# Kernel tuning notes

Hardware: AMD Instinct MI355X
Metric: run time of the kernel (lower is better)

Reference implementation:

```python
import jax, jax.numpy as jnp
import numpy as np

E, H, F, LE, LD, K, CD, DIN = 256, 8, 1024, 4, 3, 8, 4, 4
B, S = 16, 512
SIG2 = 1.0 ** 2 + 1e-8   # dr_sigma**2 + 1e-8
EPS = 1e-5               # LayerNorm / BatchNorm eps


def _ln(x, w, b):
    m = x.mean(-1, keepdims=True)
    v = ((x - m) ** 2).mean(-1, keepdims=True)
    return (x - m) / jnp.sqrt(v + EPS) * w + b


def _gelu(x):
    return jax.nn.gelu(x, approximate=False)  # torch nn.GELU default = exact erf


def _mha(xq, xkv, qkv_w, qkv_b, out_w, out_b, bias=None):
    # torch nn.MultiheadAttention (batch_first), additive float attn bias broadcast over heads
    wq, wk, wv = jnp.split(qkv_w, 3, axis=0)
    bq, bk, bv = jnp.split(qkv_b, 3)
    q = xq @ wq.T + bq
    k = xkv @ wk.T + bk
    v = xkv @ wv.T + bv
    Bn, Tq, Tk = q.shape[0], q.shape[1], k.shape[1]
    hd = E // H
    qh = q.reshape(Bn, Tq, H, hd)
    kh = k.reshape(Bn, Tk, H, hd)
    vh = v.reshape(Bn, Tk, H, hd)
    s = jnp.einsum('bqhd,bkhd->bhqk', qh, kh) / jnp.sqrt(jnp.asarray(hd, q.dtype))
    if bias is not None:
        s = s + bias[:, None]  # same bias for every head
    p = jax.nn.softmax(s, axis=-1)
    o = jnp.einsum('bhqk,bkhd->bqhd', p, vh).reshape(Bn, Tq, E)
    return o @ out_w.T + out_b


def _forward(x, mask, parent_idx, in_w, in_b, bn_w, bn_b, dr_gamma,
             e_qkv_w, e_qkv_b, e_out_w, e_out_b, e_l1_w, e_l1_b, e_l2_w, e_l2_b,
             e_n1_w, e_n1_b, e_n2_w, e_n2_b,
             parent_w, parent_b, query_embed, c1_w, c1_b, c2_w, c2_b,
             d_sqkv_w, d_sqkv_b, d_sout_w, d_sout_b,
             d_cqkv_w, d_cqkv_b, d_cout_w, d_cout_b,
             d_l1_w, d_l1_b, d_l2_w, d_l2_b,
             d_n1_w, d_n1_b, d_n2_w, d_n2_b, d_n3_w, d_n3_b,
             child_w, child_b, o1_w, o1_b, o2_w, o2_b):
    x = jnp.nan_to_num(x)
    # input_dim==4 convention: (log_pt, dEta, dPhi, log_E)
    coords = jnp.stack([x[..., 1], x[..., 2]], axis=-1)          # [B,S,2]
    # input_proj: Linear -> BatchNorm1d (eval: mean 0, var 1) -> GELU (dropout=identity in eval)
    h = x @ in_w.T + in_b
    h = (h / jnp.sqrt(1.0 + EPS)) * bn_w + bn_b
    h = _gelu(h)
    # dR Gaussian attention bias: [B,S,S]; mask is all-valid so no -inf fill
    d = coords[:, :, None, :] - coords[:, None, :, :]
    dr2 = d[..., 0] ** 2 + d[..., 1] ** 2
    bias = -(dr_gamma[0] * dr2) / (2.0 * SIG2)
    # dR-biased pre-norm encoder
    for i in range(LE):
        hn = _ln(h, e_n1_w[i], e_n1_b[i])
        h = h + _mha(hn, hn, e_qkv_w[i], e_qkv_b[i], e_out_w[i], e_out_b[i], bias)
        hn = _ln(h, e_n2_w[i], e_n2_b[i])
        h = h + _gelu(hn @ e_l1_w[i].T + e_l1_b[i]) @ e_l2_w[i].T + e_l2_b[i]
    memory = jnp.nan_to_num(h)
    parent_logit = (memory @ parent_w.T + parent_b)[..., 0]       # [B,S]
    # conditional decoder queries
    p = memory[jnp.arange(memory.shape[0]), parent_idx]           # [B,E]
    m = mask.astype(memory.dtype)
    g = (memory * m[..., None]).sum(1) / jnp.maximum(m.sum(1, keepdims=True), 1.0)
    cond = _gelu(jnp.concatenate([p, g], -1) @ c1_w.T + c1_b) @ c2_w.T + c2_b
    t = query_embed[None] + cond[:, None]                         # [B,K,E]
    # pre-norm transformer decoder (self-attn, cross-attn, ff)
    for i in range(LD):
        tn = _ln(t, d_n1_w[i], d_n1_b[i])
        t = t + _mha(tn, tn, d_sqkv_w[i], d_sqkv_b[i], d_sout_w[i], d_sout_b[i])
        tn = _ln(t, d_n2_w[i], d_n2_b[i])
        t = t + _mha(tn, memory, d_cqkv_w[i], d_cqkv_b[i], d_cout_w[i], d_cout_b[i])
        tn = _ln(t, d_n3_w[i], d_n3_b[i])
        t = t + _gelu(tn @ d_l1_w[i].T + d_l1_b[i]) @ d_l2_w[i].T + d_l2_b[i]
    child_feat = t @ child_w.T + child_b                          # [B,K,CD]
    obj_logit = (_gelu(t @ o1_w.T + o1_b) @ o2_w.T + o2_b)[..., 0]  # [B,K]
    return parent_logit, child_feat, obj_logit


def setup_inputs() -> dict:
    key = jax.random.key(0)
    ks = iter(jax.random.split(key, 64))
    def w(shape, scale=0.05):
        return jax.random.normal(next(ks), shape, jnp.float32) * scale
    return {
        'x': jax.random.normal(next(ks), (B, S, DIN), jnp.float32),
        'mask': jnp.ones((B, S), dtype=bool),
        'parent_idx': jax.random.randint(next(ks), (B,), 0, S),
        'in_w': w((E, DIN)), 'in_b': jnp.zeros((E,)),
        'bn_w': jnp.ones((E,)), 'bn_b': jnp.zeros((E,)),
        'dr_gamma': jnp.ones((1,)),
        'e_qkv_w': w((LE, 3 * E, E)), 'e_qkv_b': jnp.zeros((LE, 3 * E)),
        'e_out_w': w((LE, E, E)), 'e_out_b': jnp.zeros((LE, E)),
        'e_l1_w': w((LE, F, E)), 'e_l1_b': jnp.zeros((LE, F)),
        'e_l2_w': w((LE, E, F)), 'e_l2_b': jnp.zeros((LE, E)),
        'e_n1_w': jnp.ones((LE, E)), 'e_n1_b': jnp.zeros((LE, E)),
        'e_n2_w': jnp.ones((LE, E)), 'e_n2_b': jnp.zeros((LE, E)),
        'parent_w': w((1, E)), 'parent_b': jnp.zeros((1,)),
        'query_embed': w((K, E), 0.02),
        'c1_w': w((E, 2 * E)), 'c1_b': jnp.zeros((E,)),
        'c2_w': w((E, E)), 'c2_b': jnp.zeros((E,)),
        'd_sqkv_w': w((LD, 3 * E, E)), 'd_sqkv_b': jnp.zeros((LD, 3 * E)),
        'd_sout_w': w((LD, E, E)), 'd_sout_b': jnp.zeros((LD, E)),
        'd_cqkv_w': w((LD, 3 * E, E)), 'd_cqkv_b': jnp.zeros((LD, 3 * E)),
        'd_cout_w': w((LD, E, E)), 'd_cout_b': jnp.zeros((LD, E)),
        'd_l1_w': w((LD, F, E)), 'd_l1_b': jnp.zeros((LD, F)),
        'd_l2_w': w((LD, E, F)), 'd_l2_b': jnp.zeros((LD, E)),
        'd_n1_w': jnp.ones((LD, E)), 'd_n1_b': jnp.zeros((LD, E)),
        'd_n2_w': jnp.ones((LD, E)), 'd_n2_b': jnp.zeros((LD, E)),
        'd_n3_w': jnp.ones((LD, E)), 'd_n3_b': jnp.zeros((LD, E)),
        'child_w': w((CD, E)), 'child_b': jnp.zeros((CD,)),
        'o1_w': w((E, E)), 'o1_b': jnp.zeros((E,)),
        'o2_w': w((1, E)), 'o2_b': jnp.zeros((1,)),
    }


def reference(x, mask, parent_idx, in_w, in_b, bn_w, bn_b, dr_gamma,
              e_qkv_w, e_qkv_b, e_out_w, e_out_b, e_l1_w, e_l1_b, e_l2_w, e_l2_b,
              e_n1_w, e_n1_b, e_n2_w, e_n2_b,
              parent_w, parent_b, query_embed, c1_w, c1_b, c2_w, c2_b,
              d_sqkv_w, d_sqkv_b, d_sout_w, d_sout_b,
              d_cqkv_w, d_cqkv_b, d_cout_w, d_cout_b,
              d_l1_w, d_l1_b, d_l2_w, d_l2_b,
              d_n1_w, d_n1_b, d_n2_w, d_n2_b, d_n3_w, d_n3_b,
              child_w, child_b, o1_w, o1_b, o2_w, o2_b):
    return _forward(x, mask, parent_idx, in_w, in_b, bn_w, bn_b, dr_gamma,
                    e_qkv_w, e_qkv_b, e_out_w, e_out_b, e_l1_w, e_l1_b, e_l2_w, e_l2_b,
                    e_n1_w, e_n1_b, e_n2_w, e_n2_b,
                    parent_w, parent_b, query_embed, c1_w, c1_b, c2_w, c2_b,
                    d_sqkv_w, d_sqkv_b, d_sout_w, d_sout_b,
                    d_cqkv_w, d_cqkv_b, d_cout_w, d_cout_b,
                    d_l1_w, d_l1_b, d_l2_w, d_l2_b,
                    d_n1_w, d_n1_b, d_n2_w, d_n2_b, d_n3_w, d_n3_b,
                    child_w, child_b, o1_w, o1_b, o2_w, o2_b)
```

## Files before the change

### kernel.cpp

```cpp
#include <hip/hip_runtime.h>
#include <math.h>

#define E 256
#define H 8
#define HD 32
#define FF 1024
#define LE 4
#define LDN 3
#define KQ 8
#define CDIM 4
#define DIN 4
#define BATCH 16
#define SEQ 512

typedef __attribute__((ext_vector_type(8))) short s8b;
typedef __attribute__((ext_vector_type(4))) float f32x4;

__device__ __forceinline__ float gelu_f(float x) {
  return 0.5f * x * (1.f + erff(x * 0.70710678118654752f));
}

__device__ __forceinline__ unsigned short f2b(float f) {
  union { float f; unsigned u; } a;
  a.f = f;
  unsigned r = (a.u + 0x7fffu + ((a.u >> 16) & 1u)) >> 16;
  return (unsigned short)r;
}

__device__ __forceinline__ float b2f(unsigned short u) {
  union { unsigned u; float f; } a;
  a.u = ((unsigned)u) << 16;
  return a.f;
}

__device__ __forceinline__ void gload16(const unsigned short* g, unsigned short* l) {
  __builtin_amdgcn_global_load_lds((const __attribute__((address_space(1))) void*)g,
                                   (__attribute__((address_space(3))) void*)l, 16, 0, 0);
}

template <int GELU, int RESID, int OMODE>
__global__ __launch_bounds__(256) void mfma_gemm_kernel(
    const unsigned short* __restrict__ A, const unsigned short* __restrict__ Wt,
    const float* __restrict__ bias, const float* __restrict__ resid,
    float* __restrict__ outf, unsigned short* __restrict__ outb,
    unsigned short* __restrict__ vtb,
    int M, int N, int K) {
  __shared__ __align__(16) unsigned short As[128 * 32];
  __shared__ __align__(16) unsigned short Bs[128 * 32];
  int tid = threadIdx.x;
  int lane = tid & 63, w = tid >> 6;
  int row0 = blockIdx.y * 128, col0 = blockIdx.x * 128;
  int wr = (w >> 1) * 64, wc = (w & 1) * 64;
  f32x4 acc[4][4] = {};

  int sr0 = w * 32 + (lane >> 2);
  int sr1 = sr0 + 16;
  int sc = lane & 3;
  int gc0 = (sc ^ ((sr0 >> 1) & 3)) * 8;
  int gc1 = (sc ^ ((sr1 >> 1) & 3)) * 8;
  const unsigned short* Ap0 = A + (size_t)(row0 + sr0) * K + gc0;
  const unsigned short* Ap1 = A + (size_t)(row0 + sr1) * K + gc1;
  const unsigned short* Bp0 = Wt + (size_t)(col0 + sr0) * K + gc0;
  const unsigned short* Bp1 = Wt + (size_t)(col0 + sr1) * K + gc1;
  unsigned short* lA0 = As + (w * 32) * 32;
  unsigned short* lA1 = As + (w * 32 + 16) * 32;
  unsigned short* lB0 = Bs + (w * 32) * 32;
  unsigned short* lB1 = Bs + (w * 32 + 16) * 32;

  for (int k0 = 0; k0 < K; k0 += 32) {
    __syncthreads();
    gload16(Ap0 + k0, lA0);
    gload16(Ap1 + k0, lA1);
    gload16(Bp0 + k0, lB0);
    gload16(Bp1 + k0, lB1);
    __syncthreads();
    int krow = lane & 15, kq = lane >> 4;
    s8b afr[4], bfr[4];
    #pragma unroll
    for (int mi = 0; mi < 4; ++mi) {
      int r = wr + mi * 16 + krow;
      afr[mi] = *(const s8b*)(As + r * 32 + ((kq ^ ((r >> 1) & 3)) * 8));
    }
    #pragma unroll
    for (int ni = 0; ni < 4; ++ni) {
      int r = wc + ni * 16 + krow;
      bfr[ni] = *(const s8b*)(Bs + r * 32 + ((kq ^ ((r >> 1) & 3)) * 8));
    }
    #pragma unroll
    for (int mi = 0; mi < 4; ++mi)
      #pragma unroll
      for (int ni = 0; ni < 4; ++ni)
        acc[mi][ni] = __builtin_amdgcn_mfma_f32_16x16x32_bf16(afr[mi], bfr[ni], acc[mi][ni], 0, 0, 0);
  }

  int cl = lane & 15, rb = (lane >> 4) * 4;
  #pragma unroll
  for (int ni = 0; ni < 4; ++ni) {
    int col = col0 + wc + ni * 16 + cl;
    float bv = bias[col];
    #pragma unroll
    for (int mi = 0; mi < 4; ++mi) {
      #pragma unroll
      for (int j = 0; j < 4; ++j) {
        int row = row0 + wr + mi * 16 + rb + j;
        float v = acc[mi][ni][j] + bv;
        if (RESID) v += resid[(size_t)row * N + col];
        if (GELU) v = gelu_f(v);
        if (OMODE == 0) {
          outf[(size_t)row * N + col] = v;
        } else if (OMODE == 1) {
          outb[(size_t)row * N + col] = f2b(v);
        } else {
          int b = row >> 9, s = row & 511;
          int sect = col >> 8, hh = (col >> 5) & 7, d = col & 31;
          if (sect < 2)
            outb[((((size_t)sect * BATCH + b) * H + hh) * SEQ + s) * HD + d] = f2b(v);
          else
            vtb[(((size_t)b * H + hh) * HD + d) * SEQ + s] = f2b(v);
        }
      }
    }
  }
}

__global__ __launch_bounds__(256) void mfma_attn_kernel(
    const unsigned short* __restrict__ qkb, const unsigned short* __restrict__ vt,
    const float2* __restrict__ carr, const float* __restrict__ gamma_p,
    unsigned short* __restrict__ out) {
  __shared__ __align__(16) unsigned short P[4][16 * 64];
  int tid = threadIdx.x, lane = tid & 63, w = tid >> 6;
  int qt = blockIdx.x, h = blockIdx.y, b = blockIdx.z;
  int q0 = qt * 64 + w * 16;
  const unsigned short* qh = qkb + (((size_t)b * H + h) * SEQ) * HD;
  const unsigned short* kh = qkb + ((((size_t)BATCH + b) * H + h) * SEQ) * HD;
  const unsigned short* vh = vt + (((size_t)b * H + h) * HD) * SEQ;
  int r16 = lane & 15, q4 = lane >> 4;
  s8b qa = *(const s8b*)(qh + (size_t)(q0 + r16) * HD + q4 * 8);
  float eq[4], pq[4];
  #pragma unroll
  for (int j = 0; j < 4; ++j) {
    float2 c = carr[b * SEQ + q0 + q4 * 4 + j];
    eq[j] = c.x; pq[j] = c.y;
  }
  float gam = gamma_p[0] * 0.49999999500000004f;
  const float scale = 0.17677669529663687f;
  float m[4], lsum[4];
  #pragma unroll
  for (int j = 0; j < 4; ++j) { m[j] = -1e30f; lsum[j] = 0.f; }
  f32x4 o0 = {}, o1 = {};
  const f32x4 zf = {0.f, 0.f, 0.f, 0.f};
  unsigned short* pw = &P[w][0];

  for (int t = 0; t < SEQ / 64; ++t) {
    int k0 = t * 64;
    f32x4 sf[4];
    #pragma unroll
    for (int f = 0; f < 4; ++f) {
      s8b bk = *(const s8b*)(kh + (size_t)(k0 + f * 16 + r16) * HD + q4 * 8);
      sf[f] = __builtin_amdgcn_mfma_f32_16x16x32_bf16(qa, bk, zf, 0, 0, 0);
    }
    float ek[4], pk[4];
    #pragma unroll
    for (int f = 0; f < 4; ++f) {
      float2 c = carr[b * SEQ + k0 + f * 16 + r16];
      ek[f] = c.x; pk[f] = c.y;
    }
    float sc_[4][4];
    float tmax[4] = {-1e30f, -1e30f, -1e30f, -1e30f};
    #pragma unroll
    for (int f = 0; f < 4; ++f)
      #pragma unroll
      for (int j = 0; j < 4; ++j) {
        float de = eq[j] - ek[f], dp = pq[j] - pk[f];
        float v = sf[f][j] * scale - gam * (de * de + dp * dp);
        sc_[f][j] = v;
        tmax[j] = fmaxf(tmax[j], v);
      }
    #pragma unroll
    for (int j = 0; j < 4; ++j) {
      #pragma unroll
      for (int off = 1; off < 16; off <<= 1)
        tmax[j] = fmaxf(tmax[j], __shfl_xor(tmax[j], off));
      float mn = fmaxf(m[j], tmax[j]);
      float al = __expf(m[j] - mn);
      m[j] = mn;
      lsum[j] *= al;
      o0[j] *= al;
      o1[j] *= al;
    }
    __syncthreads();
    #pragma unroll
    for (int f = 0; f < 4; ++f)
      #pragma unroll
      for (int j = 0; j < 4; ++j) {
        float p = __expf(sc_[f][j] - m[j]);
        lsum[j] += p;
        int prow = q4 * 4 + j;
        int c = f * 16 + r16;
        int chunk = (c >> 3) ^ (prow & 7);
        pw[prow * 64 + chunk * 8 + (c & 7)] = f2b(p);
      }
    __syncthreads();
    #pragma unroll
    for (int ks = 0; ks < 2; ++ks) {
      int chunk = (ks * 4 + q4) ^ (r16 & 7);
      s8b pa = *(const s8b*)(pw + r16 * 64 + chunk * 8);
      s8b v0 = *(const s8b*)(vh + (size_t)r16 * SEQ + k0 + ks * 32 + q4 * 8);
      s8b v1 = *(const s8b*)(vh + (size_t)(16 + r16) * SEQ + k0 + ks * 32 + q4 * 8);
      o0 = __builtin_amdgcn_mfma_f32_16x16x32_bf16(pa, v0, o0, 0, 0, 0);
      o1 = __builtin_amdgcn_mfma_f32_16x16x32_bf16(pa, v1, o1, 0, 0, 0);
    }
  }
  #pragma unroll
  for (int j = 0; j < 4; ++j) {
    #pragma unroll
    for (int off = 1; off < 16; off <<= 1)
      lsum[j] += __shfl_xor(lsum[j], off);
    float inv = 1.f / lsum[j];
    size_t rbase = ((size_t)(b * SEQ + q0 + q4 * 4 + j)) * E + h * HD;
    out[rbase + r16] = f2b(o0[j] * inv);
    out[rbase + 16 + r16] = f2b(o1[j] * inv);
  }
}

__global__ void coords_kernel(const float* __restrict__ x, float2* __restrict__ carr) {
  int i = blockIdx.x * 256 + threadIdx.x;
  if (i >= BATCH * SEQ) return;
  carr[i] = make_float2(x[(size_t)i * DIN + 1], x[(size_t)i * DIN + 2]);
}

__global__ void f2b_kernel(const float* __restrict__ in, unsigned short* __restrict__ out, int n4) {
  int i = blockIdx.x * 256 + threadIdx.x;
  if (i >= n4) return;
  float4 v = ((const float4*)in)[i];
  ushort4 o;
  o.x = f2b(v.x); o.y = f2b(v.y); o.z = f2b(v.z); o.w = f2b(v.w);
  ((ushort4*)out)[i] = o;
}

__global__ void kvw_remap_kernel(const float* __restrict__ w, const float* __restrict__ b,
                                 unsigned short* __restrict__ wout, float* __restrict__ bout) {
  int i = blockIdx.x * 256 + threadIdx.x;
  if (i < 1536) bout[i] = b[(i >> 9) * 768 + 256 + (i & 511)];
  if (i >= 98304) return;
  int row = i >> 6, cc = i & 63;
  int l = row >> 9, rr = row & 511;
  const float* src = w + ((size_t)l * 768 + 256 + rr) * 256 + cc * 4;
  float4 v = *(const float4*)src;
  ushort4 o;
  o.x = f2b(v.x); o.y = f2b(v.y); o.z = f2b(v.z); o.w = f2b(v.w);
  *(ushort4*)(wout + (size_t)row * 256 + cc * 4) = o;
}


template <int N, int GELU>
__global__ __launch_bounds__(256) void dec_ln_gemv_kernel(
    const float* __restrict__ t, const float* __restrict__ nw, const float* __restrict__ nb,
    const float* __restrict__ W, const float* __restrict__ bias, float* __restrict__ outg) {
  __shared__ float X[8][256];
  __shared__ float Pp[4][64][9];
  int b = blockIdx.x, by = blockIdx.y, tid = threadIdx.x;
  const float* tg = t + (size_t)b * 2048;
  int w = tid >> 6, l = tid & 63;
  #pragma unroll
  for (int rr = 0; rr < 2; ++rr) {
    int r = w * 2 + rr;
    float v0 = tg[r * 256 + l], v1 = tg[r * 256 + 64 + l];
    float v2 = tg[r * 256 + 128 + l], v3 = tg[r * 256 + 192 + l];
    float s = v0 + v1 + v2 + v3;
    for (int o = 32; o > 0; o >>= 1) s += __shfl_xor(s, o);
    float mean = s * (1.f / 256);
    float d0 = v0 - mean, d1 = v1 - mean, d2 = v2 - mean, d3 = v3 - mean;
    float var = d0 * d0 + d1 * d1 + d2 * d2 + d3 * d3;
    for (int o = 32; o > 0; o >>= 1) var += __shfl_xor(var, o);
    float inv = rsqrtf(var * (1.f / 256) + 1e-5f);
    X[r][l] = d0 * inv * nw[l] + nb[l];
    X[r][l + 64] = d1 * inv * nw[l + 64] + nb[l + 64];
    X[r][l + 128] = d2 * inv * nw[l + 128] + nb[l + 128];
    X[r][l + 192] = d3 * inv * nw[l + 192] + nb[l + 192];
  }
  __syncthreads();
  int j = tid & 63, kq = tid >> 6;
  int col = by * 64 + j;
  const float4* wp = (const float4*)(W + (size_t)col * 256 + kq * 64);
  float acc[8] = {};
  #pragma unroll
  for (int kk = 0; kk < 16; ++kk) {
    float4 wv = wp[kk];
    int base = kq * 64 + kk * 4;
    #pragma unroll
    for (int r = 0; r < 8; ++r) {
      float4 xv = *(const float4*)&X[r][base];
      acc[r] += xv.x * wv.x + xv.y * wv.y + xv.z * wv.z + xv.w * wv.w;
    }
  }
  #pragma unroll
  for (int r = 0; r < 8; ++r) Pp[kq][j][r] = acc[r];
  __syncthreads();
  for (int i = tid; i < 512; i += 256) {
    int r = i & 7, j2 = i >> 3;
    float v = Pp[0][j2][r] + Pp[1][j2][r] + Pp[2][j2][r] + Pp[3][j2][r] + bias[by * 64 + j2];
    if (GELU) v = gelu_f(v);
    outg[((size_t)b * 8 + r) * N + by * 64 + j2] = v;
  }
}

__global__ __launch_bounds__(256) void dec_gemv_resid_kernel(
    const float* __restrict__ Xg, const float* __restrict__ W, const float* __restrict__ bias,
    float* __restrict__ t) {
  __shared__ float X[8][256];
  __shared__ float Pp[4][64][9];
  int b = blockIdx.x, by = blockIdx.y, tid = threadIdx.x;
  const float* xg = Xg + (size_t)b * 2048;
  for (int i = tid; i < 2048; i += 256) ((float*)X)[i] = xg[i];
  __syncthreads();
  int j = tid & 63, kq = tid >> 6;
  int col = by * 64 + j;
  const float4* wp = (const float4*)(W + (size_t)col * 256 + kq * 64);
  float acc[8] = {};
  #pragma unroll
  for (int kk = 0; kk < 16; ++kk) {
    float4 wv = wp[kk];
    int base = kq * 64 + kk * 4;
    #pragma unroll
    for (int r = 0; r < 8; ++r) {
      float4 xv = *(const float4*)&X[r][base];
      acc[r] += xv.x * wv.x + xv.y * wv.y + xv.z * wv.z + xv.w * wv.w;
    }
  }
  #pragma unroll
  for (int r = 0; r < 8; ++r) Pp[kq][j][r] = acc[r];
  __syncthreads();
  for (int i = tid; i < 512; i += 256) {
    int r = i & 7, j2 = i >> 3;
    float v = Pp[0][j2][r] + Pp[1][j2][r] + Pp[2][j2][r] + Pp[3][j2][r] + bias[by * 64 + j2];
    t[((size_t)b * 8 + r) * 256 + by * 64 + j2] += v;
  }
}

__global__ __launch_bounds__(256) void dec_ffn2_kernel(
    const float* __restrict__ MIDg, const float* __restrict__ W, const float* __restrict__ bias,
    float* __restrict__ t) {
  __shared__ float X[8][1024];
  __shared__ float Pp[4][64][9];
  int b = blockIdx.x, by = blockIdx.y, tid = threadIdx.x;
  const float* xg = MIDg + (size_t)b * 8192;
  for (int i = tid; i < 8192; i += 256) ((float*)X)[i] = xg[i];
  __syncthreads();
  int j = tid & 63, kq = tid >> 6;
  int col = by * 64 + j;
  const float4* wp = (const float4*)(W + (size_t)col * 1024 + kq * 256);
  float acc[8] = {};
  #pragma unroll 8
  for (int kk = 0; kk < 64; ++kk) {
    float4 wv = wp[kk];
    int base = kq * 256 + kk * 4;
    #pragma unroll
    for (int r = 0; r < 8; ++r) {
      float4 xv = *(const float4*)&X[r][base];
      acc[r] += xv.x * wv.x + xv.y * wv.y + xv.z * wv.z + xv.w * wv.w;
    }
  }
  #pragma unroll
  for (int r = 0; r < 8; ++r) Pp[kq][j][r] = acc[r];
  __syncthreads();
  for (int i = tid; i < 512; i += 256) {
    int r = i & 7, j2 = i >> 3;
    float v = Pp[0][j2][r] + Pp[1][j2][r] + Pp[2][j2][r] + Pp[3][j2][r] + bias[by * 64 + j2];
    t[((size_t)b * 8 + r) * 256 + by * 64 + j2] += v;
  }
}

__global__ __launch_bounds__(256) void dec_selfattn_kernel(
    const float* __restrict__ qkvg, float* __restrict__ ao) {
  __shared__ float QK[8][768];
  __shared__ float S[512];
  int b = blockIdx.x, tid = threadIdx.x;
  const float* qg = qkvg + (size_t)b * 8 * 768;
  for (int i = tid; i < 6144; i += 256) ((float*)QK)[i] = qg[i];
  __syncthreads();
  for (int t2 = tid; t2 < 512; t2 += 256) {
    int h = t2 >> 6, q = (t2 >> 3) & 7, k = t2 & 7;
    const float* qp = &QK[q][h * 32];
    const float* kp = &QK[k][256 + h * 32];
    float d = 0.f;
    #pragma unroll
    for (int jj = 0; jj < 32; ++jj) d += qp[jj] * kp[jj];
    S[t2] = d * 0.17677669529663687f;
  }
  __syncthreads();
  if (tid < 64) {
    float* row = &S[tid * 8];
    float m = row[0];
    #pragma unroll
    for (int k = 1; k < 8; ++k) m = fmaxf(m, row[k]);
    float sum = 0.f;
    #pragma unroll
    for (int k = 0; k < 8; ++k) { float e = __expf(row[k] - m); row[k] = e; sum += e; }
    float inv = 1.f / sum;
    #pragma unroll
    for (int k = 0; k < 8; ++k) row[k] *= inv;
  }
  __syncthreads();
  for (int i = tid; i < 2048; i += 256) {
    int q = i >> 8, c = i & 255, h = c >> 5;
    const float* pr = &S[h * 64 + q * 8];
    float acc = 0.f;
    #pragma unroll
    for (int k = 0; k < 8; ++k) acc += pr[k] * QK[k][512 + c];
    ao[(size_t)b * 2048 + i] = acc;
  }
}

__global__ __launch_bounds__(256) void cross_attn_kernel(
    const float* __restrict__ Q, const unsigned short* __restrict__ KV,
    int koff, int voff, float* __restrict__ out) {
  __shared__ float sv[512];
  __shared__ float red[256];
  __shared__ float qv[32];
  __shared__ float pvred[8][32];
  int tid = threadIdx.x;
  int bid = blockIdx.x;
  int q = bid % KQ;
  int h = (bid / KQ) % H;
  int b = bid / (KQ * H);
  if (tid < 32) qv[tid] = Q[((size_t)(b * KQ + q)) * E + h * HD + tid];
  __syncthreads();
  const float scale = 0.17677669529663687f;
  for (int k = tid; k < SEQ; k += 256) {
    const unsigned short* kp = KV + ((size_t)(b * SEQ + k)) * 1536 + koff + h * HD;
    float d = 0.f;
    #pragma unroll
    for (int j4 = 0; j4 < 4; ++j4) {
      s8b kv8 = *(const s8b*)(kp + j4 * 8);
      #pragma unroll
      for (int j = 0; j < 8; ++j)
        d += qv[j4 * 8 + j] * b2f((unsigned short)kv8[j]);
    }
    sv[k] = d * scale;
  }
  __syncthreads();
  float m = -1e30f;
  for (int k = tid; k < SEQ; k += 256) m = fmaxf(m, sv[k]);
  red[tid] = m; __syncthreads();
  for (int s = 128; s > 0; s >>= 1) {
    if (tid < s) red[tid] = fmaxf(red[tid], red[tid + s]);
    __syncthreads();
  }
  m = red[0]; __syncthreads();
  float lsum = 0.f;
  for (int k = tid; k < SEQ; k += 256) { float e = __expf(sv[k] - m); sv[k] = e; lsum += e; }
  red[tid] = lsum; __syncthreads();
  for (int s = 128; s > 0; s >>= 1) {
    if (tid < s) red[tid] += red[tid + s];
    __syncthreads();
  }
  float denom = red[0];
  int d = tid & 31, g = tid >> 5;
  float acc = 0.f;
  for (int k = g; k < SEQ; k += 8)
    acc += sv[k] * b2f(KV[((size_t)(b * SEQ + k)) * 1536 + voff + h * HD + d]);
  pvred[g][d] = acc;
  __syncthreads();
  if (tid < 32) {
    float r = 0.f;
    #pragma unroll
    for (int gg = 0; gg < 8; ++gg) r += pvred[gg][tid];
    out[((size_t)(b * KQ + q)) * E + h * HD + tid] = r / denom;
  }
}

__global__ void ln_bf16_kernel(const float* __restrict__ in, const float* __restrict__ w,
                               const float* __restrict__ b, unsigned short* __restrict__ out) {
  int r = blockIdx.x;
  int l = threadIdx.x;
  const float* p = in + (size_t)r * E;
  float v0 = p[l], v1 = p[l + 64], v2 = p[l + 128], v3 = p[l + 192];
  float s = v0 + v1 + v2 + v3;
  for (int off = 32; off > 0; off >>= 1) s += __shfl_xor(s, off);
  float mean = s * (1.f / E);
  float d0 = v0 - mean, d1 = v1 - mean, d2 = v2 - mean, d3 = v3 - mean;
  float var = d0 * d0 + d1 * d1 + d2 * d2 + d3 * d3;
  for (int off = 32; off > 0; off >>= 1) var += __shfl_xor(var, off);
  float inv = rsqrtf(var * (1.f / E) + 1e-5f);
  unsigned short* o = out + (size_t)r * E;
  o[l]       = f2b(d0 * inv * w[l]       + b[l]);
  o[l + 64]  = f2b(d1 * inv * w[l + 64]  + b[l + 64]);
  o[l + 128] = f2b(d2 * inv * w[l + 128] + b[l + 128]);
  o[l + 192] = f2b(d3 * inv * w[l + 192] + b[l + 192]);
}

__global__ void input_proj_kernel(const float* __restrict__ x, const float* __restrict__ in_w,
                                  const float* __restrict__ in_b, const float* __restrict__ bn_w,
                                  const float* __restrict__ bn_b, float* __restrict__ h) {
  int idx = blockIdx.x * 256 + threadIdx.x;
  int row = idx >> 8, e = idx & 255;
  const float* xr = x + (size_t)row * DIN;
  float v = in_b[e];
  #pragma unroll
  for (int i = 0; i < DIN; ++i) v += xr[i] * in_w[e * DIN + i];
  v = v * (1.0f / sqrtf(1.0f + 1e-5f)) * bn_w[e] + bn_b[e];
  h[idx] = gelu_f(v);
}

__global__ __launch_bounds__(256) void pool_gather_kernel(
    const float* __restrict__ mem, const int* __restrict__ pidx, float* __restrict__ pg) {
  __shared__ float red[8][32];
  int b = blockIdx.x, cy = blockIdx.y, tid = threadIdx.x;
  int c = cy * 32 + (tid & 31), g = tid >> 5;
  float s = 0.f;
  for (int r = g; r < SEQ; r += 8)
    s += mem[((size_t)b * SEQ + r) * E + c];
  red[g][tid & 31] = s;
  __syncthreads();
  if (tid < 32) {
    float t = 0.f;
    #pragma unroll
    for (int g2 = 0; g2 < 8; ++g2) t += red[g2][tid];
    pg[(size_t)b * 512 + 256 + cy * 32 + tid] = t * (1.f / SEQ);
    pg[(size_t)b * 512 + cy * 32 + tid] = mem[((size_t)b * SEQ + pidx[b]) * E + cy * 32 + tid];
  }
}

__global__ void cond_kernel(const float* __restrict__ pg, const float* __restrict__ c1w,
                            const float* __restrict__ c1b, const float* __restrict__ c2w,
                            const float* __restrict__ c2b, const float* __restrict__ qe,
                            float* __restrict__ t) {
  __shared__ float PG[512];
  __shared__ float C1[256];
  int b = blockIdx.x, c = threadIdx.x;
  PG[c] = pg[(size_t)b * 512 + c];
  PG[c + 256] = pg[(size_t)b * 512 + 256 + c];
  __syncthreads();
  const float4* wp = (const float4*)(c1w + (size_t)c * 512);
  float acc = c1b[c];
  #pragma unroll 8
  for (int kk = 0; kk < 128; ++kk) {
    float4 wv = wp[kk];
    int base = kk * 4;
    acc += PG[base] * wv.x + PG[base + 1] * wv.y + PG[base + 2] * wv.z + PG[base + 3] * wv.w;
  }
  C1[c] = gelu_f(acc);
  __syncthreads();
  const float4* wp2 = (const float4*)(c2w + (size_t)c * 256);
  float acc2 = c2b[c];
  #pragma unroll 8
  for (int kk = 0; kk < 64; ++kk) {
    float4 wv = wp2[kk];
    int base = kk * 4;
    acc2 += C1[base] * wv.x + C1[base + 1] * wv.y + C1[base + 2] * wv.z + C1[base + 3] * wv.w;
  }
  #pragma unroll
  for (int k = 0; k < KQ; ++k)
    t[((size_t)b * KQ + k) * E + c] = qe[k * E + c] + acc2;
}

__global__ void head_kernel(const float* __restrict__ t,
                            const float* __restrict__ childw, const float* __restrict__ childb,
                            const float* __restrict__ o1w, const float* __restrict__ o1b,
                            const float* __restrict__ o2w, const float* __restrict__ o2b,
                            float* __restrict__ out_child, float* __restrict__ out_obj) {
  __shared__ float tr[256];
  __shared__ float red[256];
  int r = blockIdx.x, c = threadIdx.x;
  tr[c] = t[(size_t)r * E + c];
  __syncthreads();
  const float4* wp = (const float4*)(o1w + (size_t)c * 256);
  float acc = o1b[c];
  #pragma unroll 8
  for (int kk = 0; kk < 64; ++kk) {
    float4 wv = wp[kk];
    int base = kk * 4;
    acc += tr[base] * wv.x + tr[base + 1] * wv.y + tr[base + 2] * wv.z + tr[base + 3] * wv.w;
  }
  red[c] = gelu_f(acc) * o2w[c];
  __syncthreads();
  for (int s = 128; s > 0; s >>= 1) {
    if (c < s) red[c] += red[c + s];
    __syncthreads();
  }
  if (c == 0) out_obj[r] = red[0] + o2b[0];
  __syncthreads();
  #pragma unroll
  for (int j = 0; j < CDIM; ++j) {
    red[c] = tr[c] * childw[j * E + c];
    __syncthreads();
    for (int s = 128; s > 0; s >>= 1) {
      if (c < s) red[c] += red[c + s];
      __syncthreads();
    }
    if (c == 0) out_child[r * CDIM + j] = red[0] + childb[j];
    __syncthreads();
  }
}

__global__ void rowdot_kernel(const float* __restrict__ A, const float* __restrict__ w,
                              const float* __restrict__ bias, float* __restrict__ out) {
  int r = blockIdx.x, l = threadIdx.x;
  const float* p = A + (size_t)r * E;
  float s = p[l] * w[l] + p[l + 64] * w[l + 64] + p[l + 128] * w[l + 128] + p[l + 192] * w[l + 192];
  for (int off = 32; off > 0; off >>= 1) s += __shfl_xor(s, off);
  if (l == 0) out[r] = s + bias[0];
}

extern "C" void kernel_launch(void* const* d_in, const int* in_sizes, int n_in,
                              void* d_out, int out_size, void* d_ws, size_t ws_size,
                              hipStream_t stream) {
  const float* x          = (const float*)d_in[0];
  const int*   parent_idx = (const int*)d_in[2];
  const float* in_w  = (const float*)d_in[3];
  const float* in_b  = (const float*)d_in[4];
  const float* bn_w  = (const float*)d_in[5];
  const float* bn_b  = (const float*)d_in[6];
  const float* dr_gamma = (const float*)d_in[7];
  const float* e_qkv_w = (const float*)d_in[8];
  const float* e_qkv_b = (const float*)d_in[9];
  const float* e_out_w = (const float*)d_in[10];
  const float* e_out_b = (const float*)d_in[11];
  const float* e_l1_w = (const float*)d_in[12];
  const float* e_l1_b = (const float*)d_in[13];
  const float* e_l2_w = (const float*)d_in[14];
  const float* e_l2_b = (const float*)d_in[15];
  const float* e_n1_w = (const float*)d_in[16];
  const float* e_n1_b = (const float*)d_in[17];
  const float* e_n2_w = (const float*)d_in[18];
  const float* e_n2_b = (const float*)d_in[19];
  const float* parent_w = (const float*)d_in[20];
  const float* parent_b = (const float*)d_in[21];
  const float* query_embed = (const float*)d_in[22];
  const float* c1_w = (const float*)d_in[23];
  const float* c1_b = (const float*)d_in[24];
  const float* c2_w = (const float*)d_in[25];
  const float* c2_b = (const float*)d_in[26];
  const float* d_sqkv_w = (const float*)d_in[27];
  const float* d_sqkv_b = (const float*)d_in[28];
  const float* d_sout_w = (const float*)d_in[29];
  const float* d_sout_b = (const float*)d_in[30];
  const float* d_cqkv_w = (const float*)d_in[31];
  const float* d_cqkv_b = (const float*)d_in[32];
  const float* d_cout_w = (const float*)d_in[33];
  const float* d_cout_b = (const float*)d_in[34];
  const float* d_l1_w = (const float*)d_in[35];
  const float* d_l1_b = (const float*)d_in[36];
  const float* d_l2_w = (const float*)d_in[37];
  const float* d_l2_b = (const float*)d_in[38];
  const float* d_n1_w = (const float*)d_in[39];
  const float* d_n1_b = (const float*)d_in[40];
  const float* d_n2_w = (const float*)d_in[41];
  const float* d_n2_b = (const float*)d_in[42];
  const float* d_n3_w = (const float*)d_in[43];
  const float* d_n3_b = (const float*)d_in[44];
  const float* child_w = (const float*)d_in[45];
  const float* child_b = (const float*)d_in[46];
  const float* o1_w = (const float*)d_in[47];
  const float* o1_b = (const float*)d_in[48];
  const float* o2_w = (const float*)d_in[49];
  const float* o2_b = (const float*)d_in[50];

  float* out = (float*)d_out;
  const int ROWS = BATCH * SEQ;
  const int TROWS = BATCH * KQ;

  float* ws = (float*)d_ws;
  float* h         = ws;
  float* attnout_d = h + (size_t)ROWS * E;
  float* pg        = attnout_d + (size_t)TROWS * E;
  float* tbuf      = pg + BATCH * 2 * E;
  float* q_t       = tbuf + (size_t)TROWS * E;
  float* qkv_t     = q_t + (size_t)TROWS * E;
  float* dmid      = qkv_t + (size_t)TROWS * 3 * E;
  float* kvb3      = dmid + (size_t)TROWS * FF;
  unsigned short* kv_bf   = (unsigned short*)(kvb3 + 1536);
  unsigned short* hn_bf   = kv_bf + (size_t)ROWS * 1536;
  unsigned short* attn_bf = hn_bf + (size_t)ROWS * E;
  unsigned short* mid_bf  = attn_bf + (size_t)ROWS * E;
  unsigned short* eqkv_bf = mid_bf + (size_t)ROWS * FF;
  unsigned short* eout_bf = eqkv_bf + (size_t)LE * 3 * E * E;
  unsigned short* el1_bf  = eout_bf + (size_t)LE * E * E;
  unsigned short* el2_bf  = el1_bf + (size_t)LE * FF * E;
  unsigned short* kvw_bf  = el2_bf + (size_t)LE * E * FF;
  float2* carr = (float2*)(kvw_bf + (size_t)1536 * 256);
  unsigned short* qkb = mid_bf;
  unsigned short* vtb = mid_bf + (size_t)2 * ROWS * E;

  auto cvt = [&](const float* src, unsigned short* dst, size_t n) {
    int n4 = (int)(n / 4);
    f2b_kernel<<<(n4 + 255) / 256, 256, 0, stream>>>(src, dst, n4);
  };

  cvt(e_qkv_w, eqkv_bf, (size_t)LE * 3 * E * E);
  cvt(e_out_w, eout_bf, (size_t)LE * E * E);
  cvt(e_l1_w, el1_bf, (size_t)LE * FF * E);
  cvt(e_l2_w, el2_bf, (size_t)LE * E * FF);
  kvw_remap_kernel<<<384, 256, 0, stream>>>(d_cqkv_w, d_cqkv_b, kvw_bf, kvb3);
  coords_kernel<<<(BATCH * SEQ + 255) / 256, 256, 0, stream>>>(x, carr);

  input_proj_kernel<<<ROWS, 256, 0, stream>>>(x, in_w, in_b, bn_w, bn_b, h);

  for (int i = 0; i < LE; ++i) {
    const float* qb = e_qkv_b + (size_t)i * 3 * E;
    const float* ob = e_out_b + (size_t)i * E;
    const float* l1b = e_l1_b + (size_t)i * FF;
    const float* l2b = e_l2_b + (size_t)i * E;
    ln_bf16_kernel<<<ROWS, 64, 0, stream>>>(h, e_n1_w + i * E, e_n1_b + i * E, hn_bf);
    mfma_gemm_kernel<0, 0, 2><<<dim3(6, 64), 256, 0, stream>>>(
        hn_bf, eqkv_bf + (size_t)i * 3 * E * E, qb, nullptr, nullptr, qkb, vtb, ROWS, 3 * E, E);
    mfma_attn_kernel<<<dim3(SEQ / 64, H, BATCH), 256, 0, stream>>>(qkb, vtb, carr, dr_gamma, attn_bf);
    mfma_gemm_kernel<0, 1, 0><<<dim3(2, 64), 256, 0, stream>>>(
        attn_bf, eout_bf + (size_t)i * E * E, ob, h, h, nullptr, nullptr, ROWS, E, E);
    ln_bf16_kernel<<<ROWS, 64, 0, stream>>>(h, e_n2_w + i * E, e_n2_b + i * E, hn_bf);
    mfma_gemm_kernel<1, 0, 1><<<dim3(8, 64), 256, 0, stream>>>(
        hn_bf, el1_bf + (size_t)i * FF * E, l1b, nullptr, nullptr, mid_bf, nullptr, ROWS, FF, E);
    mfma_gemm_kernel<0, 1, 0><<<dim3(2, 64), 256, 0, stream>>>(
        mid_bf, el2_bf + (size_t)i * E * FF, l2b, h, h, nullptr, nullptr, ROWS, E, FF);
  }

  rowdot_kernel<<<ROWS, 64, 0, stream>>>(h, parent_w, parent_b, out);

  pool_gather_kernel<<<dim3(BATCH, 8), 256, 0, stream>>>(h, parent_idx, pg);
  cond_kernel<<<BATCH, 256, 0, stream>>>(pg, c1_w, c1_b, c2_w, c2_b, query_embed, tbuf);

  cvt(h, hn_bf, (size_t)ROWS * E);
  mfma_gemm_kernel<0, 0, 1><<<dim3(12, 64), 256, 0, stream>>>(
      hn_bf, kvw_bf, kvb3, nullptr, nullptr, kv_bf, nullptr, ROWS, 3 * E * 2, E);

  for (int i = 0; i < LDN; ++i) {
    dec_ln_gemv_kernel<768, 0><<<dim3(BATCH, 12), 256, 0, stream>>>(
        tbuf, d_n1_w + i * E, d_n1_b + i * E,
        d_sqkv_w + (size_t)i * 3 * E * E, d_sqkv_b + (size_t)i * 3 * E, qkv_t);
    dec_selfattn_kernel<<<BATCH, 256, 0, stream>>>(qkv_t, attnout_d);
    dec_gemv_resid_kernel<<<dim3(BATCH, 4), 256, 0, stream>>>(
        attnout_d, d_sout_w + (size_t)i * E * E, d_sout_b + (size_t)i * E, tbuf);
    dec_ln_gemv_kernel<256, 0><<<dim3(BATCH, 4), 256, 0, stream>>>(
        tbuf, d_n2_w + i * E, d_n2_b + i * E,
        d_cqkv_w + (size_t)i * 3 * E * E, d_cqkv_b + (size_t)i * 3 * E, q_t);
    cross_attn_kernel<<<BATCH * H * KQ, 256, 0, stream>>>(
        q_t, kv_bf, i * 512, i * 512 + 256, attnout_d);
    dec_gemv_resid_kernel<<<dim3(BATCH, 4), 256, 0, stream>>>(
        attnout_d, d_cout_w + (size_t)i * E * E, d_cout_b + (size_t)i * E, tbuf);
    dec_ln_gemv_kernel<1024, 1><<<dim3(BATCH, 16), 256, 0, stream>>>(
        tbuf, d_n3_w + i * E, d_n3_b + i * E,
        d_l1_w + (size_t)i * FF * E, d_l1_b + (size_t)i * FF, dmid);
    dec_ffn2_kernel<<<dim3(BATCH, 4), 256, 0, stream>>>(
        dmid, d_l2_w + (size_t)i * E * FF, d_l2_b + (size_t)i * E, tbuf);
  }

  head_kernel<<<TROWS, 256, 0, stream>>>(tbuf, child_w, child_b, o1_w, o1_b, o2_w, o2_b,
                                         out + ROWS, out + ROWS + TROWS * CDIM);
}
```

Before: 833.3 us.

## Fuse LayerNorm into encoder GEMMs and decoder self-attention into output projection

Adds a GEMM kernel that computes the LayerNorm of each 128-row block directly into shared memory as bf16 (full K=256 resident) before running the MFMA loop. This removes the separate ln_bf16 launches and the bf16 round trip through global memory for both the QKV and FFN1 GEMMs. In the decoder, self-attention is fused with the output-projection GEMV plus residual, so each of the 4 column blocks recomputes the tiny attention. The cost is redundant LN work across column blocks, larger LDS use (64KB A tile), and repeated attention compute.

```diff
diff --git a/kernel.cpp b/kernel.cpp
--- a/kernel.cpp
+++ b/kernel.cpp
@@ -123,6 +123,103 @@
   }
 }
 
+template <int GELU, int OMODE>
+__global__ __launch_bounds__(256) void mfma_gemm_ln_kernel(
+    const float* __restrict__ hsrc, const float* __restrict__ nw, const float* __restrict__ nb,
+    const unsigned short* __restrict__ Wt, const float* __restrict__ bias,
+    unsigned short* __restrict__ outb, unsigned short* __restrict__ vtb, int N) {
+  __shared__ __align__(16) unsigned short As[128 * 256];
+  __shared__ __align__(16) unsigned short Bs[128 * 32];
+  int tid = threadIdx.x;
+  int lane = tid & 63, w = tid >> 6;
+  int row0 = blockIdx.y * 128, col0 = blockIdx.x * 128;
+  int wr = (w >> 1) * 64, wc = (w & 1) * 64;
+  f32x4 acc[4][4] = {};
+
+  for (int rr = 0; rr < 32; ++rr) {
+    int r = w * 32 + rr;
+    float4 v = *(const float4*)(hsrc + (size_t)(row0 + r) * 256 + lane * 4);
+    float s = v.x + v.y + v.z + v.w;
+    #pragma unroll
+    for (int o = 32; o > 0; o >>= 1) s += __shfl_xor(s, o);
+    float mean = s * (1.f / 256);
+    float d0 = v.x - mean, d1 = v.y - mean, d2 = v.z - mean, d3 = v.w - mean;
+    float var = d0 * d0 + d1 * d1 + d2 * d2 + d3 * d3;
+    #pragma unroll
+    for (int o = 32; o > 0; o >>= 1) var += __shfl_xor(var, o);
+    float inv = rsqrtf(var * (1.f / 256) + 1e-5f);
+    int c0 = lane * 4;
+    ushort4 ov;
+    ov.x = f2b(d0 * inv * nw[c0] + nb[c0]);
+    ov.y = f2b(d1 * inv * nw[c0 + 1] + nb[c0 + 1]);
+    ov.z = f2b(d2 * inv * nw[c0 + 2] + nb[c0 + 2]);
+    ov.w = f2b(d3 * inv * nw[c0 + 3] + nb[c0 + 3]);
+    int chunkp = (lane >> 1) ^ (r & 7);
+    *(ushort4*)(As + r * 256 + chunkp * 8 + (lane & 1) * 4) = ov;
+  }
+
+  int sr0 = w * 32 + (lane >> 2);
+  int sr1 = sr0 + 16;
+  int sc = lane & 3;
+  int gc0 = (sc ^ ((sr0 >> 1) & 3)) * 8;
+  int gc1 = (sc ^ ((sr1 >> 1) & 3)) * 8;
+  const unsigned short* Bp0 = Wt + (size_t)(col0 + sr0) * 256 + gc0;
+  const unsigned short* Bp1 = Wt + (size_t)(col0 + sr1) * 256 + gc1;
+  unsigned short* lB0 = Bs + (w * 32) * 32;
+  unsigned short* lB1 = Bs + (w * 32 + 16) * 32;
+
+  for (int k0 = 0; k0 < 256; k0 += 32) {
+    __syncthreads();
+    gload16(Bp0 + k0, lB0);
+    gload16(Bp1 + k0, lB1);
+    __syncthreads();
+    int krow = lane & 15, kq = lane >> 4;
+    int cb = (k0 >> 3) + kq;
+    s8b afr[4], bfr[4];
+    #pragma unroll
+    for (int mi = 0; mi < 4; ++mi) {
+      int r = wr + mi * 16 + krow;
+      afr[mi] = *(const s8b*)(As + r * 256 + ((cb ^ (r & 7)) * 8));
+    }
+    #pragma unroll
+    for (int ni = 0; ni < 4; ++ni) {
+      int r = wc + ni * 16 + krow;
+      bfr[ni] = *(const s8b*)(Bs + r * 32 + ((kq ^ ((r >> 1) & 3)) * 8));
+    }
+    #pragma unroll
+    for (int mi = 0; mi < 4; ++mi)
+      #pragma unroll
+      for (int ni = 0; ni < 4; ++ni)
+        acc[mi][ni] = __builtin_amdgcn_mfma_f32_16x16x32_bf16(afr[mi], bfr[ni], acc[mi][ni], 0, 0, 0);
+  }
+
+  int cl = lane & 15, rb = (lane >> 4) * 4;
+  #pragma unroll
+  for (int ni = 0; ni < 4; ++ni) {
+    int col = col0 + wc + ni * 16 + cl;
+    float bv = bias[col];
+    #pragma unroll
+    for (int mi = 0; mi < 4; ++mi) {
+      #pragma unroll
+      for (int j = 0; j < 4; ++j) {
+        int row = row0 + wr + mi * 16 + rb + j;
+        float v = acc[mi][ni][j] + bv;
+        if (GELU) v = gelu_f(v);
+        if (OMODE == 1) {
+          outb[(size_t)row * N + col] = f2b(v);
+        } else {
+          int b = row >> 9, s = row & 511;
+          int sect = col >> 8, hh = (col >> 5) & 7, d = col & 31;
+          if (sect < 2)
+            outb[((((size_t)sect * BATCH + b) * H + hh) * SEQ + s) * HD + d] = f2b(v);
+          else
+            vtb[(((size_t)b * H + hh) * HD + d) * SEQ + s] = f2b(v);
+        }
+      }
+    }
+  }
+}
+
 __global__ __launch_bounds__(256) void mfma_attn_kernel(
     const unsigned short* __restrict__ qkb, const unsigned short* __restrict__ vt,
     const float2* __restrict__ carr, const float* __restrict__ gamma_p,
@@ -305,6 +402,73 @@
   }
 }
 
+__global__ __launch_bounds__(256) void dec_selfattn_sout_kernel(
+    const float* __restrict__ qkvg, const float* __restrict__ W, const float* __restrict__ bias,
+    float* __restrict__ t) {
+  __shared__ float QK[8][768];
+  __shared__ float S[512];
+  __shared__ float X[8][256];
+  __shared__ float Pp[4][64][9];
+  int b = blockIdx.x, by = blockIdx.y, tid = threadIdx.x;
+  const float* qg = qkvg + (size_t)b * 8 * 768;
+  for (int i = tid; i < 6144; i += 256) ((float*)QK)[i] = qg[i];
+  __syncthreads();
+  for (int t2 = tid; t2 < 512; t2 += 256) {
+    int h = t2 >> 6, q = (t2 >> 3) & 7, k = t2 & 7;
+    const float* qp = &QK[q][h * 32];
+    const float* kp = &QK[k][256 + h * 32];
+    float d = 0.f;
+    #pragma unroll
+    for (int jj = 0; jj < 32; ++jj) d += qp[jj] * kp[jj];
+    S[t2] = d * 0.17677669529663687f;
+  }
+  __syncthreads();
+  if (tid < 64) {
+    float* row = &S[tid * 8];
+    float m = row[0];
+    #pragma unroll
+    for (int k = 1; k < 8; ++k) m = fmaxf(m, row[k]);
+    float sum = 0.f;
+    #pragma unroll
+    for (int k = 0; k < 8; ++k) { float e = __expf(row[k] - m); row[k] = e; sum += e; }
+    float inv = 1.f / sum;
+    #pragma unroll
+    for (int k = 0; k < 8; ++k) row[k] *= inv;
+  }
+  __syncthreads();
+  for (int i = tid; i < 2048; i += 256) {
+    int q = i >> 8, c = i & 255, h = c >> 5;
+    const float* pr = &S[h * 64 + q * 8];
+    float acc = 0.f;
+    #pragma unroll
+    for (int k = 0; k < 8; ++k) acc += pr[k] * QK[k][512 + c];
+    X[q][c] = acc;
+  }
+  __syncthreads();
+  int j = tid & 63, kq = tid >> 6;
+  int col = by * 64 + j;
+  const float4* wp = (const float4*)(W + (size_t)col * 256 + kq * 64);
+  float acc[8] = {};
+  #pragma unroll
+  for (int kk = 0; kk < 16; ++kk) {
+    float4 wv = wp[kk];
+    int base = kq * 64 + kk * 4;
+    #pragma unroll
+    for (int r = 0; r < 8; ++r) {
+      float4 xv = *(const float4*)&X[r][base];
+      acc[r] += xv.x * wv.x + xv.y * wv.y + xv.z * wv.z + xv.w * wv.w;
+    }
+  }
+  #pragma unroll
+  for (int r = 0; r < 8; ++r) Pp[kq][j][r] = acc[r];
+  __syncthreads();
+  for (int i = tid; i < 512; i += 256) {
+    int r = i & 7, j2 = i >> 3;
+    float v = Pp[0][j2][r] + Pp[1][j2][r] + Pp[2][j2][r] + Pp[3][j2][r] + bias[by * 64 + j2];
+    t[((size_t)b * 8 + r) * 256 + by * 64 + j2] += v;
+  }
+}
+
 __global__ __launch_bounds__(256) void dec_gemv_resid_kernel(
     const float* __restrict__ Xg, const float* __restrict__ W, const float* __restrict__ bias,
     float* __restrict__ t) {
@@ -368,47 +532,6 @@
     int r = i & 7, j2 = i >> 3;
     float v = Pp[0][j2][r] + Pp[1][j2][r] + Pp[2][j2][r] + Pp[3][j2][r] + bias[by * 64 + j2];
     t[((size_t)b * 8 + r) * 256 + by * 64 + j2] += v;
-  }
-}
-
-__global__ __launch_bounds__(256) void dec_selfattn_kernel(
-    const float* __restrict__ qkvg, float* __restrict__ ao) {
-  __shared__ float QK[8][768];
-  __shared__ float S[512];
-  int b = blockIdx.x, tid = threadIdx.x;
-  const float* qg = qkvg + (size_t)b * 8 * 768;
-  for (int i = tid; i < 6144; i += 256) ((float*)QK)[i] = qg[i];
-  __syncthreads();
-  for (int t2 = tid; t2 < 512; t2 += 256) {
-    int h = t2 >> 6, q = (t2 >> 3) & 7, k = t2 & 7;
-    const float* qp = &QK[q][h * 32];
-    const float* kp = &QK[k][256 + h * 32];
-    float d = 0.f;
-    #pragma unroll
-    for (int jj = 0; jj < 32; ++jj) d += qp[jj] * kp[jj];
-    S[t2] = d * 0.17677669529663687f;
-  }
-  __syncthreads();
-  if (tid < 64) {
-    float* row = &S[tid * 8];
-    float m = row[0];
-    #pragma unroll
-    for (int k = 1; k < 8; ++k) m = fmaxf(m, row[k]);
-    float sum = 0.f;
-    #pragma unroll
-    for (int k = 0; k < 8; ++k) { float e = __expf(row[k] - m); row[k] = e; sum += e; }
-    float inv = 1.f / sum;
-    #pragma unroll
-    for (int k = 0; k < 8; ++k) row[k] *= inv;
-  }
-  __syncthreads();
-  for (int i = tid; i < 2048; i += 256) {
-    int q = i >> 8, c = i & 255, h = c >> 5;
-    const float* pr = &S[h * 64 + q * 8];
-    float acc = 0.f;
-    #pragma unroll
-    for (int k = 0; k < 8; ++k) acc += pr[k] * QK[k][512 + c];
-    ao[(size_t)b * 2048 + i] = acc;
   }
 }
 
@@ -468,26 +591,6 @@
     for (int gg = 0; gg < 8; ++gg) r += pvred[gg][tid];
     out[((size_t)(b * KQ + q)) * E + h * HD + tid] = r / denom;
   }
-}
-
-__global__ void ln_bf16_kernel(const float* __restrict__ in, const float* __restrict__ w,
-                               const float* __restrict__ b, unsigned short* __restrict__ out) {
-  int r = blockIdx.x;
-  int l = threadIdx.x;
-  const float* p = in + (size_t)r * E;
-  float v0 = p[l], v1 = p[l + 64], v2 = p[l + 128], v3 = p[l + 192];
-  float s = v0 + v1 + v2 + v3;
-  for (int off = 32; off > 0; off >>= 1) s += __shfl_xor(s, off);
-  float mean = s * (1.f / E);
-  float d0 = v0 - mean, d1 = v1 - mean, d2 = v2 - mean, d3 = v3 - mean;
-  float var = d0 * d0 + d1 * d1 + d2 * d2 + d3 * d3;
-  for (int off = 32; off > 0; off >>= 1) var += __shfl_xor(var, off);
-  float inv = rsqrtf(var * (1.f / E) + 1e-5f);
-  unsigned short* o = out + (size_t)r * E;
-  o[l]       = f2b(d0 * inv * w[l]       + b[l]);
-  o[l + 64]  = f2b(d1 * inv * w[l + 64]  + b[l + 64]);
-  o[l + 128] = f2b(d2 * inv * w[l + 128] + b[l + 128]);
-  o[l + 192] = f2b(d3 * inv * w[l + 192] + b[l + 192]);
 }
 
 __global__ void input_proj_kernel(const float* __restrict__ x, const float* __restrict__ in_w,
@@ -702,15 +805,15 @@
     const float* ob = e_out_b + (size_t)i * E;
     const float* l1b = e_l1_b + (size_t)i * FF;
     const float* l2b = e_l2_b + (size_t)i * E;
-    ln_bf16_kernel<<<ROWS, 64, 0, stream>>>(h, e_n1_w + i * E, e_n1_b + i * E, hn_bf);
-    mfma_gemm_kernel<0, 0, 2><<<dim3(6, 64), 256, 0, stream>>>(
-        hn_bf, eqkv_bf + (size_t)i * 3 * E * E, qb, nullptr, nullptr, qkb, vtb, ROWS, 3 * E, E);
+    mfma_gemm_ln_kernel<0, 2><<<dim3(6, 64), 256, 0, stream>>>(
+        h, e_n1_w + i * E, e_n1_b + i * E,
+        eqkv_bf + (size_t)i * 3 * E * E, qb, qkb, vtb, 3 * E);
     mfma_attn_kernel<<<dim3(SEQ / 64, H, BATCH), 256, 0, stream>>>(qkb, vtb, carr, dr_gamma, attn_bf);
     mfma_gemm_kernel<0, 1, 0><<<dim3(2, 64), 256, 0, stream>>>(
         attn_bf, eout_bf + (size_t)i * E * E, ob, h, h, nullptr, nullptr, ROWS, E, E);
-    ln_bf16_kernel<<<ROWS, 64, 0, stream>>>(h, e_n2_w + i * E, e_n2_b + i * E, hn_bf);
-    mfma_gemm_kernel<1, 0, 1><<<dim3(8, 64), 256, 0, stream>>>(
-        hn_bf, el1_bf + (size_t)i * FF * E, l1b, nullptr, nullptr, mid_bf, nullptr, ROWS, FF, E);
+    mfma_gemm_ln_kernel<1, 1><<<dim3(8, 64), 256, 0, stream>>>(
+        h, e_n2_w + i * E, e_n2_b + i * E,
+        el1_bf + (size_t)i * FF * E, l1b, mid_bf, nullptr, FF);
     mfma_gemm_kernel<0, 1, 0><<<dim3(2, 64), 256, 0, stream>>>(
         mid_bf, el2_bf + (size_t)i * E * FF, l2b, h, h, nullptr, nullptr, ROWS, E, FF);
   }
@@ -728,9 +831,8 @@
     dec_ln_gemv_kernel<768, 0><<<dim3(BATCH, 12), 256, 0, stream>>>(
         tbuf, d_n1_w + i * E, d_n1_b + i * E,
         d_sqkv_w + (size_t)i * 3 * E * E, d_sqkv_b + (size_t)i * 3 * E, qkv_t);
-    dec_selfattn_kernel<<<BATCH, 256, 0, stream>>>(qkv_t, attnout_d);
-    dec_gemv_resid_kernel<<<dim3(BATCH, 4), 256, 0, stream>>>(
-        attnout_d, d_sout_w + (size_t)i * E * E, d_sout_b + (size_t)i * E, tbuf);
+    dec_selfattn_sout_kernel<<<dim3(BATCH, 4), 256, 0, stream>>>(
+        qkv_t, d_sout_w + (size_t)i * E * E, d_sout_b + (size_t)i * E, tbuf);
     dec_ln_gemv_kernel<256, 0><<<dim3(BATCH, 4), 256, 0, stream>>>(
         tbuf, d_n2_w + i * E, d_n2_b + i * E,
         d_cqkv_w + (size_t)i * 3 * E * E, d_cqkv_b + (size_t)i * 3 * E, q_t);
```

Result: slower. 946.5 us (+13.6%).
